# Kernel tuning notes

Hardware: AMD Instinct MI355X
Metric: run time of the kernel (lower is better)

## Reference

```python
import jax, jax.numpy as jnp
import numpy as np


def setup_inputs() -> dict:
    key = jax.random.key(0)
    ks = jax.random.split(key, 5)
    B, T, C, HS = 8, 2048, 1024, 64
    return {
        "x_q": jax.random.normal(ks[0], (B, T, C), dtype=jnp.float32),
        "x_kv": jax.random.normal(ks[1], (B, T, C), dtype=jnp.float32),
        "Wq": jax.random.normal(ks[2], (C, HS), dtype=jnp.float32) * (C ** -0.5),
        "Wk": jax.random.normal(ks[3], (C, HS), dtype=jnp.float32) * (C ** -0.5),
        "Wv": jax.random.normal(ks[4], (C, HS), dtype=jnp.float32) * (C ** -0.5),
    }


def reference(x_q, x_kv, Wq, Wk, Wv):
    # x_q, x_kv: [B, T, C]; W*: [C, HS]
    B, T, C = x_q.shape
    q = jnp.einsum("btc,ch->bth", x_q, Wq)   # [B, T, HS]
    k = jnp.einsum("btc,ch->bth", x_kv, Wk)  # [B, T, HS]
    v = jnp.einsum("btc,ch->bth", x_kv, Wv)  # [B, T, HS]
    # NOTE: original scales by d_model**-0.5 (C), not head_size**-0.5
    wei = jnp.einsum("bqh,bkh->bqk", q, k) * (C ** -0.5)  # [B, T, T]
    causal = jnp.tril(jnp.ones((T, T), dtype=bool))
    wei = jnp.where(causal, wei, -jnp.inf)
    wei = jax.nn.softmax(wei, axis=-1)
    out = jnp.einsum("bqk,bkh->bqh", wei, v)  # [B, T, HS]
    return out
```

## Files before the change

kernel.cpp:

```cpp
#include <hip/hip_runtime.h>

typedef __bf16 bf16_t;
typedef __bf16 bf16x8 __attribute__((ext_vector_type(8)));
typedef float f32x4 __attribute__((ext_vector_type(4)));
typedef unsigned short u16x4 __attribute__((ext_vector_type(4)));

#define B_ 8
#define T_ 2048
#define C_ 1024
#define HS_ 64
#define VSTRIDE 2080

#define MFMA __builtin_amdgcn_mfma_f32_16x16x32_bf16

__device__ __forceinline__ float fast_exp2(float x) {
#if __has_builtin(__builtin_amdgcn_exp2f)
  return __builtin_amdgcn_exp2f(x);
#else
  return exp2f(x);
#endif
}

__device__ __forceinline__ void async_ld16(const void* gsrc, void* lds_dst) {
  __builtin_amdgcn_global_load_lds(
      (const __attribute__((address_space(1))) void*)gsrc,
      (__attribute__((address_space(3))) void*)lds_dst, 16, 0, 0);
}

__global__ __launch_bounds__(256) void repack_w(
    const float* __restrict__ Wq, const float* __restrict__ Wk,
    const float* __restrict__ Wv, bf16_t* __restrict__ pq,
    bf16_t* __restrict__ pk, bf16_t* __restrict__ pv) {
  const float* W = (blockIdx.y == 0) ? Wq : ((blockIdx.y == 1) ? Wk : Wv);
  bf16_t* P = (blockIdx.y == 0) ? pq : ((blockIdx.y == 1) ? pk : pv);
  int t = blockIdx.x * 256 + threadIdx.x;
  int lane = t & 63, nt = (t >> 6) & 3, kc = t >> 8;
  int quad = lane >> 4, ln = lane & 15;
  bf16x8 v;
#pragma unroll
  for (int j = 0; j < 8; ++j)
    v[j] = (bf16_t)W[(kc * 32 + quad * 8 + j) * HS_ + nt * 16 + ln];
  *(bf16x8*)(P + (size_t)t * 8) = v;
}

__global__ __launch_bounds__(256) void proj_mfma(
    const float* __restrict__ xq, const float* __restrict__ xkv,
    const bf16_t* __restrict__ pq, const bf16_t* __restrict__ pk,
    const bf16_t* __restrict__ pv, bf16_t* __restrict__ q,
    bf16_t* __restrict__ k, bf16_t* __restrict__ vT) {
  __shared__ float Xb[2][64][128];
  __shared__ bf16_t Bb[2][2][16][512];

  const bool is_kv = (blockIdx.y != 0);
  const float* x = is_kv ? xkv : xq;
  const bf16_t* pA = is_kv ? pk : pq;
  const bf16_t* pB = pv;
  bf16_t* outA = is_kv ? k : q;

  const int w = threadIdx.x >> 6, lane = threadIdx.x & 63;
  const int quad = lane >> 4, ln = lane & 15;
  const int m0blk = blockIdx.x * 64;
  const int m0 = m0blk + w * 16;
  const int l32 = lane & 31, lhalf = lane >> 5;

  f32x4 acc0[4], acc1[4];
#pragma unroll
  for (int nt = 0; nt < 4; ++nt) {
    acc0[nt] = (f32x4){0.f, 0.f, 0.f, 0.f};
    acc1[nt] = (f32x4){0.f, 0.f, 0.f, 0.f};
  }

  auto STAGE = [&](int c, int buf) {
#pragma unroll
    for (int i = 0; i < 8; ++i) {
      const int row = w * 16 + 2 * i + lhalf;
      const int sg = l32 ^ (row & 7);
      async_ld16(x + (size_t)(m0blk + row) * C_ + c * 128 + sg * 4,
                 &Xb[buf][w * 16 + 2 * i][0]);
    }
#pragma unroll
    for (int j = 0; j < 4; ++j) {
      const int p = w * 4 + j;
      async_ld16(pA + (size_t)(c * 16 + p) * 512 + lane * 8,
                 &Bb[buf][0][p][0]);
    }
    if (is_kv) {
#pragma unroll
      for (int j = 0; j < 4; ++j) {
        const int p = w * 4 + j;
        async_ld16(pB + (size_t)(c * 16 + p) * 512 + lane * 8,
                   &Bb[buf][1][p][0]);
      }
    }
  };

  auto COMPUTE = [&](int buf) {
    const int swz = (ln & 7) << 4;
    const char* rp = (const char*)&Xb[buf][w * 16 + ln][0];
#pragma unroll
    for (int kc2 = 0; kc2 < 4; ++kc2) {
      f32x4 xlo = *(const f32x4*)(rp + ((kc2 * 128 + quad * 32) ^ swz));
      f32x4 xhi = *(const f32x4*)(rp + ((kc2 * 128 + quad * 32 + 16) ^ swz));
      bf16x8 a;
#pragma unroll
      for (int j = 0; j < 4; ++j) {
        a[j] = (bf16_t)xlo[j];
        a[4 + j] = (bf16_t)xhi[j];
      }
#pragma unroll
      for (int nt = 0; nt < 4; ++nt) {
        bf16x8 b0 = *(const bf16x8*)&Bb[buf][0][kc2 * 4 + nt][lane * 8];
        acc0[nt] = MFMA(a, b0, acc0[nt], 0, 0, 0);
      }
      if (is_kv) {
#pragma unroll
        for (int nt = 0; nt < 4; ++nt) {
          bf16x8 b1 = *(const bf16x8*)&Bb[buf][1][kc2 * 4 + nt][lane * 8];
          acc1[nt] = MFMA(a, b1, acc1[nt], 0, 0, 0);
        }
      }
    }
  };

#define WAIT_CHUNK()                                        \
  do {                                                      \
    if (is_kv)                                              \
      asm volatile("s_waitcnt vmcnt(16)" ::: "memory");     \
    else                                                    \
      asm volatile("s_waitcnt vmcnt(12)" ::: "memory");     \
  } while (0)

  STAGE(0, 0);
  STAGE(1, 1);
  WAIT_CHUNK();
  __builtin_amdgcn_s_barrier();
  __builtin_amdgcn_sched_barrier(0);

#pragma unroll
  for (int c = 0; c < 8; ++c) {
    COMPUTE(c & 1);
    if (c == 7) break;
    asm volatile("s_waitcnt lgkmcnt(0)" ::: "memory");
    __builtin_amdgcn_s_barrier();
    __builtin_amdgcn_sched_barrier(0);
    if (c < 6) {
      STAGE(c + 2, c & 1);
      WAIT_CHUNK();
    } else {
      asm volatile("s_waitcnt vmcnt(0)" ::: "memory");
    }
    __builtin_amdgcn_s_barrier();
    __builtin_amdgcn_sched_barrier(0);
  }
#undef WAIT_CHUNK

#pragma unroll
  for (int nt = 0; nt < 4; ++nt)
#pragma unroll
    for (int r = 0; r < 4; ++r)
      outA[(size_t)(m0 + quad * 4 + r) * HS_ + nt * 16 + ln] =
          (bf16_t)acc0[nt][r];
  if (is_kv) {
    const int bb = m0 >> 11, t0 = m0 & (T_ - 1);
#pragma unroll
    for (int nt = 0; nt < 4; ++nt) {
      u16x4 pk4;
#pragma unroll
      for (int r = 0; r < 4; ++r) {
        bf16_t h = (bf16_t)acc1[nt][r];
        pk4[r] = *(unsigned short*)&h;
      }
      *(u16x4*)((unsigned short*)vT +
                ((size_t)(bb * HS_ + nt * 16 + ln)) * VSTRIDE + t0 + quad * 4) =
          pk4;
    }
  }
}

__global__ __launch_bounds__(512, 4) void attn_mfma(
    const bf16_t* __restrict__ q, const bf16_t* __restrict__ k,
    const bf16_t* __restrict__ vT, float* __restrict__ out) {
  __shared__ bf16_t p_lds[8][16][80];
  __shared__ float o_buf[8][16][66];
  __shared__ float l_buf[8][16][17];

  const int b = blockIdx.x & 7;
  const int gq = 127 - (blockIdx.x >> 3);
  const int w = threadIdx.x >> 6, lane = threadIdx.x & 63;
  const int quad = lane >> 4, ln = lane & 15;
  const int qr0 = gq * 16;
  const size_t bt = (size_t)b * T_;
  const int td = gq >> 2;

  bf16x8 aq[2];
#pragma unroll
  for (int hc = 0; hc < 2; ++hc)
    aq[hc] = *(const bf16x8*)(q + (bt + qr0 + ln) * HS_ + hc * 32 + quad * 8);

  f32x4 o_acc[4];
  float l_part[4] = {0.f, 0.f, 0.f, 0.f};
#pragma unroll
  for (int nt = 0; nt < 4; ++nt) o_acc[nt] = (f32x4){0.f, 0.f, 0.f, 0.f};
  const float scl = 0.03125f * 1.44269504088896340736f;

  bf16x8 bk[8], bv[8];
  int t = w;
  if (t <= td) {
#pragma unroll
    for (int hc = 0; hc < 2; ++hc)
#pragma unroll
      for (int nt = 0; nt < 4; ++nt)
        bk[hc * 4 + nt] = *(const bf16x8*)(k + (bt + t * 64 + nt * 16 + ln) * HS_ +
                                           hc * 32 + quad * 8);
  }

  for (; t <= td; t += 8) {
    const int kr0 = t * 64;

#pragma unroll
    for (int kc = 0; kc < 2; ++kc)
#pragma unroll
      for (int nt = 0; nt < 4; ++nt)
        bv[kc * 4 + nt] = *(const bf16x8*)(vT +
                                           ((size_t)(b * HS_ + nt * 16 + ln)) * VSTRIDE +
                                           kr0 + kc * 32 + quad * 8);

    f32x4 s[4];
#pragma unroll
    for (int nt = 0; nt < 4; ++nt) s[nt] = (f32x4){0.f, 0.f, 0.f, 0.f};
#pragma unroll
    for (int hc = 0; hc < 2; ++hc)
#pragma unroll
      for (int nt = 0; nt < 4; ++nt)
        s[nt] = MFMA(aq[hc], bk[hc * 4 + nt], s[nt], 0, 0, 0);

    if (t + 8 <= td) {
#pragma unroll
      for (int hc = 0; hc < 2; ++hc)
#pragma unroll
        for (int nt = 0; nt < 4; ++nt)
          bk[hc * 4 + nt] = *(const bf16x8*)(k +
                                             (bt + (t + 8) * 64 + nt * 16 + ln) * HS_ +
                                             hc * 32 + quad * 8);
    }

    const bool diag = (t == td);
#pragma unroll
    for (int nt = 0; nt < 4; ++nt)
#pragma unroll
      for (int r = 0; r < 4; ++r) {
        float e = fast_exp2(s[nt][r] * scl);
        if (diag && (kr0 + nt * 16 + ln > qr0 + quad * 4 + r)) e = 0.f;
        l_part[r] += e;
        p_lds[w][quad * 4 + r][nt * 16 + ln] = (bf16_t)e;
      }

#pragma unroll
    for (int kc = 0; kc < 2; ++kc) {
      bf16x8 ap = *(const bf16x8*)&p_lds[w][ln][kc * 32 + quad * 8];
#pragma unroll
      for (int nt = 0; nt < 4; ++nt)
        o_acc[nt] = MFMA(ap, bv[kc * 4 + nt], o_acc[nt], 0, 0, 0);
    }
  }

#pragma unroll
  for (int nt = 0; nt < 4; ++nt)
#pragma unroll
    for (int r = 0; r < 4; ++r)
      o_buf[w][quad * 4 + r][nt * 16 + ln] = o_acc[nt][r];
#pragma unroll
  for (int r = 0; r < 4; ++r) l_buf[w][quad * 4 + r][ln] = l_part[r];
  __syncthreads();

#pragma unroll
  for (int rr = 0; rr < 2; ++rr) {
    const int row = w + rr * 8;
    float o = 0.f, lsum = 0.f;
#pragma unroll
    for (int ww = 0; ww < 8; ++ww) {
      o += o_buf[ww][row][lane];
      lsum += l_buf[ww][row][lane & 15];
    }
#pragma unroll
    for (int off = 1; off < 16; off <<= 1) lsum += __shfl_xor(lsum, off);
    out[(bt + qr0 + row) * HS_ + lane] = o / lsum;
  }
}

extern "C" void kernel_launch(void* const* d_in, const int* in_sizes, int n_in,
                              void* d_out, int out_size, void* d_ws,
                              size_t ws_size, hipStream_t stream) {
  (void)in_sizes; (void)n_in; (void)out_size; (void)ws_size;
  const float* xq = (const float*)d_in[0];
  const float* xkv = (const float*)d_in[1];
  const float* Wq = (const float*)d_in[2];
  const float* Wk = (const float*)d_in[3];
  const float* Wv = (const float*)d_in[4];
  float* out = (float*)d_out;

  char* ws = (char*)d_ws;
  bf16_t* q = (bf16_t*)ws;
  bf16_t* kk = (bf16_t*)(ws + (2u << 20));
  bf16_t* vT = (bf16_t*)(ws + (4u << 20));
  bf16_t* pq = (bf16_t*)(ws + (6656u << 10));
  bf16_t* pk = (bf16_t*)(ws + (6784u << 10));
  bf16_t* pv = (bf16_t*)(ws + (6912u << 10));

  repack_w<<<dim3(32, 3), 256, 0, stream>>>(Wq, Wk, Wv, pq, pk, pv);
  proj_mfma<<<dim3(256, 2), 256, 0, stream>>>(xq, xkv, pq, pk, pv, q, kk, vT);
  attn_mfma<<<dim3(1024), 512, 0, stream>>>(q, kk, vT, out);
}
```

Before: 198.2 us.

## Keep projection weights in registers and stream full-K row tiles with split-K reduction

The projection kernel now loads its bf16 weight fragments once into registers (32 bf16x8 per lane) and no longer stages them through LDS for every K chunk. Each block processes 8 sequential 16-row tiles, each streamed at full K width, with the two K halves split across wave groups and combined through a small LDS reduction. The goal is to remove the repeated weight traffic and LDS weight reads so that x streaming dominates. In exchange it uses many more registers, adds an extra barrier-backed reduction per tile, drops the LDS swizzle on x, and launches fewer, larger blocks.

```diff
diff --git a/kernel.cpp b/kernel.cpp
--- a/kernel.cpp
+++ b/kernel.cpp
@@ -43,136 +43,140 @@
   *(bf16x8*)(P + (size_t)t * 8) = v;
 }
 
-__global__ __launch_bounds__(256) void proj_mfma(
+__global__ __launch_bounds__(512, 2) void proj_mfma(
     const float* __restrict__ xq, const float* __restrict__ xkv,
     const bf16_t* __restrict__ pq, const bf16_t* __restrict__ pk,
     const bf16_t* __restrict__ pv, bf16_t* __restrict__ q,
     bf16_t* __restrict__ k, bf16_t* __restrict__ vT) {
-  __shared__ float Xb[2][64][128];
-  __shared__ bf16_t Bb[2][2][16][512];
+  __shared__ float Xb[2][16][1028];
+  __shared__ float red[2][4][4][16][4];
 
   const bool is_kv = (blockIdx.y != 0);
   const float* x = is_kv ? xkv : xq;
-  const bf16_t* pA = is_kv ? pk : pq;
-  const bf16_t* pB = pv;
-  bf16_t* outA = is_kv ? k : q;
 
   const int w = threadIdx.x >> 6, lane = threadIdx.x & 63;
   const int quad = lane >> 4, ln = lane & 15;
-  const int m0blk = blockIdx.x * 64;
-  const int m0 = m0blk + w * 16;
-  const int l32 = lane & 31, lhalf = lane >> 5;
-
-  f32x4 acc0[4], acc1[4];
-#pragma unroll
-  for (int nt = 0; nt < 4; ++nt) {
-    acc0[nt] = (f32x4){0.f, 0.f, 0.f, 0.f};
-    acc1[nt] = (f32x4){0.f, 0.f, 0.f, 0.f};
-  }
-
-  auto STAGE = [&](int c, int buf) {
-#pragma unroll
-    for (int i = 0; i < 8; ++i) {
-      const int row = w * 16 + 2 * i + lhalf;
-      const int sg = l32 ^ (row & 7);
-      async_ld16(x + (size_t)(m0blk + row) * C_ + c * 128 + sg * 4,
-                 &Xb[buf][w * 16 + 2 * i][0]);
-    }
-#pragma unroll
-    for (int j = 0; j < 4; ++j) {
-      const int p = w * 4 + j;
-      async_ld16(pA + (size_t)(c * 16 + p) * 512 + lane * 8,
-                 &Bb[buf][0][p][0]);
-    }
+  const int kh = w >> 2, nt = w & 3;
+
+  bf16x8 bfr[32];
+#pragma unroll
+  for (int j = 0; j < 16; ++j) {
+    const size_t idx = (((size_t)(kh * 16 + j) * 4 + nt) * 64 + lane) * 8;
+    bfr[j * 2] = *(const bf16x8*)((is_kv ? pk : pq) + idx);
+    if (is_kv) bfr[j * 2 + 1] = *(const bf16x8*)(pv + idx);
+  }
+
+  auto STAGE = [&](int c) {
+    const size_t g = (size_t)blockIdx.x * 8 + c;
+    const int buf = c & 1;
+#pragma unroll
+    for (int i = 0; i < 2; ++i) {
+      const int r = w * 2 + i;
+      const float* src = x + (g * 16 + r) * C_;
+#pragma unroll
+      for (int qt = 0; qt < 4; ++qt)
+        async_ld16(src + qt * 256 + lane * 4, &Xb[buf][r][qt * 256]);
+    }
+  };
+
+  auto COMPUTE = [&](int buf, f32x4& a0, f32x4& a1) {
+    const char* rp = (const char*)&Xb[buf][ln][0];
     if (is_kv) {
 #pragma unroll
-      for (int j = 0; j < 4; ++j) {
-        const int p = w * 4 + j;
-        async_ld16(pB + (size_t)(c * 16 + p) * 512 + lane * 8,
-                   &Bb[buf][1][p][0]);
+      for (int j = 0; j < 16; ++j) {
+        const int s0 = (kh * 16 + j) * 8 + quad * 2;
+        f32x4 xlo = *(const f32x4*)(rp + s0 * 16);
+        f32x4 xhi = *(const f32x4*)(rp + s0 * 16 + 16);
+        bf16x8 a;
+#pragma unroll
+        for (int jj = 0; jj < 4; ++jj) {
+          a[jj] = (bf16_t)xlo[jj];
+          a[4 + jj] = (bf16_t)xhi[jj];
+        }
+        a0 = MFMA(a, bfr[j * 2], a0, 0, 0, 0);
+        a1 = MFMA(a, bfr[j * 2 + 1], a1, 0, 0, 0);
       }
+    } else {
+#pragma unroll
+      for (int j = 0; j < 16; ++j) {
+        const int s0 = (kh * 16 + j) * 8 + quad * 2;
+        f32x4 xlo = *(const f32x4*)(rp + s0 * 16);
+        f32x4 xhi = *(const f32x4*)(rp + s0 * 16 + 16);
+        bf16x8 a;
+#pragma unroll
+        for (int jj = 0; jj < 4; ++jj) {
+          a[jj] = (bf16_t)xlo[jj];
+          a[4 + jj] = (bf16_t)xhi[jj];
+        }
+        a0 = MFMA(a, bfr[j * 2], a0, 0, 0, 0);
+      }
     }
   };
 
-  auto COMPUTE = [&](int buf) {
-    const int swz = (ln & 7) << 4;
-    const char* rp = (const char*)&Xb[buf][w * 16 + ln][0];
-#pragma unroll
-    for (int kc2 = 0; kc2 < 4; ++kc2) {
-      f32x4 xlo = *(const f32x4*)(rp + ((kc2 * 128 + quad * 32) ^ swz));
-      f32x4 xhi = *(const f32x4*)(rp + ((kc2 * 128 + quad * 32 + 16) ^ swz));
-      bf16x8 a;
-#pragma unroll
-      for (int j = 0; j < 4; ++j) {
-        a[j] = (bf16_t)xlo[j];
-        a[4 + j] = (bf16_t)xhi[j];
-      }
-#pragma unroll
-      for (int nt = 0; nt < 4; ++nt) {
-        bf16x8 b0 = *(const bf16x8*)&Bb[buf][0][kc2 * 4 + nt][lane * 8];
-        acc0[nt] = MFMA(a, b0, acc0[nt], 0, 0, 0);
-      }
-      if (is_kv) {
-#pragma unroll
-        for (int nt = 0; nt < 4; ++nt) {
-          bf16x8 b1 = *(const bf16x8*)&Bb[buf][1][kc2 * 4 + nt][lane * 8];
-          acc1[nt] = MFMA(a, b1, acc1[nt], 0, 0, 0);
-        }
-      }
-    }
-  };
-
-#define WAIT_CHUNK()                                        \
-  do {                                                      \
-    if (is_kv)                                              \
-      asm volatile("s_waitcnt vmcnt(16)" ::: "memory");     \
-    else                                                    \
-      asm volatile("s_waitcnt vmcnt(12)" ::: "memory");     \
-  } while (0)
-
-  STAGE(0, 0);
-  STAGE(1, 1);
-  WAIT_CHUNK();
+  u16x4 ow0[8], ow1[8];
+
+  STAGE(0);
+  STAGE(1);
+  asm volatile("s_waitcnt vmcnt(8)" ::: "memory");
   __builtin_amdgcn_s_barrier();
   __builtin_amdgcn_sched_barrier(0);
 
 #pragma unroll
   for (int c = 0; c < 8; ++c) {
-    COMPUTE(c & 1);
-    if (c == 7) break;
+    f32x4 acc0 = (f32x4){0.f, 0.f, 0.f, 0.f};
+    f32x4 acc1 = (f32x4){0.f, 0.f, 0.f, 0.f};
+    COMPUTE(c & 1, acc0, acc1);
+    if (kh == 1) {
+      *(f32x4*)&red[0][nt][quad][ln][0] = acc0;
+      if (is_kv) *(f32x4*)&red[1][nt][quad][ln][0] = acc1;
+    }
     asm volatile("s_waitcnt lgkmcnt(0)" ::: "memory");
     __builtin_amdgcn_s_barrier();
     __builtin_amdgcn_sched_barrier(0);
+    if (kh == 0) {
+      acc0 += *(const f32x4*)&red[0][nt][quad][ln][0];
+      if (is_kv) acc1 += *(const f32x4*)&red[1][nt][quad][ln][0];
+#pragma unroll
+      for (int r = 0; r < 4; ++r) {
+        bf16_t h0 = (bf16_t)acc0[r];
+        ow0[c][r] = *(unsigned short*)&h0;
+        bf16_t h1 = (bf16_t)acc1[r];
+        ow1[c][r] = *(unsigned short*)&h1;
+      }
+    }
+    if (c == 7) break;
     if (c < 6) {
-      STAGE(c + 2, c & 1);
-      WAIT_CHUNK();
+      STAGE(c + 2);
+      asm volatile("s_waitcnt vmcnt(8)" ::: "memory");
     } else {
       asm volatile("s_waitcnt vmcnt(0)" ::: "memory");
     }
     __builtin_amdgcn_s_barrier();
     __builtin_amdgcn_sched_barrier(0);
   }
-#undef WAIT_CHUNK
-
-#pragma unroll
-  for (int nt = 0; nt < 4; ++nt)
-#pragma unroll
-    for (int r = 0; r < 4; ++r)
-      outA[(size_t)(m0 + quad * 4 + r) * HS_ + nt * 16 + ln] =
-          (bf16_t)acc0[nt][r];
-  if (is_kv) {
-    const int bb = m0 >> 11, t0 = m0 & (T_ - 1);
-#pragma unroll
-    for (int nt = 0; nt < 4; ++nt) {
-      u16x4 pk4;
-#pragma unroll
-      for (int r = 0; r < 4; ++r) {
-        bf16_t h = (bf16_t)acc1[nt][r];
-        pk4[r] = *(unsigned short*)&h;
-      }
+
+  if (kh != 0) return;
+  if (!is_kv) {
+#pragma unroll
+    for (int c = 0; c < 8; ++c) {
+      const int R0 = (blockIdx.x * 8 + c) * 16;
+#pragma unroll
+      for (int r = 0; r < 4; ++r)
+        *((unsigned short*)q + (size_t)(R0 + quad * 4 + r) * HS_ + nt * 16 +
+          ln) = ow0[c][r];
+    }
+  } else {
+#pragma unroll
+    for (int c = 0; c < 8; ++c) {
+      const int R0 = (blockIdx.x * 8 + c) * 16;
+#pragma unroll
+      for (int r = 0; r < 4; ++r)
+        *((unsigned short*)k + (size_t)(R0 + quad * 4 + r) * HS_ + nt * 16 +
+          ln) = ow0[c][r];
+      const int bb = R0 >> 11;
+      const int t0 = (R0 & (T_ - 1)) + quad * 4;
       *(u16x4*)((unsigned short*)vT +
-                ((size_t)(bb * HS_ + nt * 16 + ln)) * VSTRIDE + t0 + quad * 4) =
-          pk4;
+                ((size_t)(bb * HS_ + nt * 16 + ln)) * VSTRIDE + t0) = ow1[c];
     }
   }
 }
@@ -308,6 +312,6 @@
   bf16_t* pv = (bf16_t*)(ws + (6912u << 10));
 
   repack_w<<<dim3(32, 3), 256, 0, stream>>>(Wq, Wk, Wv, pq, pk, pv);
-  proj_mfma<<<dim3(256, 2), 256, 0, stream>>>(xq, xkv, pq, pk, pv, q, kk, vT);
+  proj_mfma<<<dim3(128, 2), 512, 0, stream>>>(xq, xkv, pq, pk, pv, q, kk, vT);
   attn_mfma<<<dim3(1024), 512, 0, stream>>>(q, kk, vT, out);
 }
```

Result: no change. 197.3 us (-0.4%).
